# Optimization experiments

Measured on AMD Instinct MI355X. Metric: run time of the kernel, lower is better.

Reference implementation:

```python
import jax, jax.numpy as jnp
import numpy as np

HID = 256
STYLE_DIM = 64
NUM_STYLES = 8
IN_DIM = 3 + STYLE_DIM


def setup_inputs() -> dict:
    key = jax.random.key(0)
    ks = jax.random.split(key, 12)
    B, H, W = 2, 512, 512
    rgb = jax.random.uniform(ks[0], (B, 3, H, W), dtype=jnp.float32)
    style_idx = jax.random.randint(ks[1], (B,), 0, NUM_STYLES, dtype=jnp.int32)
    # style embedding table (torch init: normal std=0.01)
    emb_table = 0.01 * jax.random.normal(ks[2], (NUM_STYLES, STYLE_DIM), dtype=jnp.float32)
    # kaiming-normal (fan_in, relu gain sqrt(2)) weights stored as [in, out]
    def kaiming(k, fan_in, fan_out):
        std = np.sqrt(2.0 / fan_in)
        return std * jax.random.normal(k, (fan_in, fan_out), dtype=jnp.float32)
    W0 = kaiming(ks[3], IN_DIM, HID); b0 = jnp.zeros((HID,), jnp.float32)
    W1 = kaiming(ks[4], HID, HID);    b1 = jnp.zeros((HID,), jnp.float32)
    W2 = kaiming(ks[5], HID, HID);    b2 = jnp.zeros((HID,), jnp.float32)
    W3 = kaiming(ks[6], HID, 3);      b3 = jnp.zeros((3,), jnp.float32)
    return {"rgb": rgb, "style_idx": style_idx, "emb_table": emb_table,
            "W0": W0, "b0": b0, "W1": W1, "b1": b1,
            "W2": W2, "b2": b2, "W3": W3, "b3": b3}


def reference(rgb, style_idx, emb_table, W0, b0, W1, b1, W2, b2, W3, b3):
    B, C, H, W_ = rgb.shape  # CHW image input
    # [B,3,H,W] -> [B*H*W, 3]
    rgb_flat = jnp.transpose(rgb, (0, 2, 3, 1)).reshape(-1, 3)
    # style embedding lookup, broadcast per pixel
    emb = emb_table[style_idx]                              # [B, style_dim]
    emb = jnp.broadcast_to(emb[:, None, :], (B, H * W_, STYLE_DIM)).reshape(-1, STYLE_DIM)
    x = jnp.concatenate([rgb_flat, emb], axis=-1)           # [N, 67]
    gelu = lambda t: jax.nn.gelu(t, approximate=False)      # torch nn.GELU default (erf)
    x = gelu(x @ W0 + b0)
    x = gelu(x @ W1 + b1)
    x = gelu(x @ W2 + b2)
    out_flat = jax.nn.sigmoid(x @ W3 + b3)                  # [N, 3]
    out = out_flat.reshape(B, H, W_, 3).transpose(0, 3, 1, 2)
    return out
```

## Files before the change

kernel.cpp:

```cpp
#include <hip/hip_runtime.h>

#define HW  (512*512)

typedef _Float16 half8  __attribute__((__vector_size__(16)));
typedef _Float16 half4  __attribute__((__vector_size__(8)));
typedef _Float16 half2_t __attribute__((__vector_size__(4)));
typedef float    floatx4 __attribute__((__vector_size__(16)));
typedef float    floatx2 __attribute__((__vector_size__(8)));

__device__ __forceinline__ float gelu_f(float x){
    float x2 = x * x;
    float q  = __builtin_fmaf(x2, -0.1029432f, -2.3022079f);
    float e  = __builtin_amdgcn_exp2f(x * q);
    return x * __builtin_amdgcn_rcpf(1.0f + e);
}

__device__ __forceinline__ float sigmoid_f(float x){
    float e = __builtin_amdgcn_exp2f(-1.44269504f * x);
    return __builtin_amdgcn_rcpf(1.0f + e);
}

__device__ __forceinline__ float glut_eval(const float* gl, float x){
    float p = __builtin_fmaf(x, 128.0f, 1024.0f);
    p = fminf(fmaxf(p, 0.0f), 2040.0f);
    unsigned off = ((unsigned)p) & 0xFFFFFFF8u;
    floatx2 ab = *(const floatx2*)((const char*)gl + off);
    return __builtin_fmaf(ab[0], x, ab[1]);
}


__global__ void prep_all(const float* __restrict__ W1, const float* __restrict__ W2,
                         const float* __restrict__ W3, const float* __restrict__ emb,
                         const int* __restrict__ sidx, const float* __restrict__ W0,
                         const float* __restrict__ b0,
                         _Float16* __restrict__ wp, float* __restrict__ c0){
    __shared__ float ld[32][68];
    int blk = blockIdx.x;
    int tid = threadIdx.x;
    if (blk < 64){
        int mat = blk >> 5;
        int g   = blk & 31;
        int ks  = g >> 2;
        int ntq = g & 3;
        const float* W = mat ? W2 : W1;
        int row = tid >> 3;
        int c8  = (tid & 7) * 8;
        const float* src = &W[(ks*32 + row)*256 + ntq*64 + c8];
        *(floatx4*)&ld[row][c8]     = *(const floatx4*)src;
        *(floatx4*)&ld[row][c8 + 4] = *(const floatx4*)(src + 4);
        __syncthreads();
        int lane = tid & 63;
        int nt_l = tid >> 6;
        half8 h;
        #pragma unroll
        for (int j = 0; j < 8; j++)
            h[j] = (_Float16)ld[(lane >> 4)*8 + j][nt_l*16 + (lane & 15)];
        _Float16* dst = wp + mat*65536 + (ks*16 + ntq*4 + nt_l)*512 + lane*8;
        *(half8*)dst = h;
    } else if (blk < 80){
        int i    = (blk - 64)*256 + tid;
        int j    = i & 7;
        int lane = (i >> 3) & 63;
        int ks   = i >> 9;
        int k = ks*32 + ((lane >> 4) << 3) + j;
        int n = lane & 15;
        wp[131072 + i] = (_Float16)((n < 3) ? W3[k*3 + n] : 0.0f);
    } else {
        int b = blk - 80;
        int s = sidx[b];
        float acc = b0[tid];
        #pragma unroll 8
        for (int d = 0; d < 64; d++)
            acc = fmaf(emb[s*64 + d], W0[(3 + d)*256 + tid], acc);
        c0[b*256 + tid] = acc;
    }
}

__global__ __launch_bounds__(256, 4)
void nilut_main(const float* __restrict__ rgb,
                const float* __restrict__ W0,
                const float* __restrict__ b1v,
                const float* __restrict__ b2v,
                const float* __restrict__ b3v,
                const _Float16* __restrict__ wp,
                const float* __restrict__ c0,
                float* __restrict__ out){
    __shared__ __align__(16) _Float16 act[64 * 256];
    __shared__ __align__(16) float    w0s[1024];
    __shared__ __align__(16) float    rgbs[192];
    __shared__ __align__(16) float    glut[512];

    const int tid = threadIdx.x;
    const int wg  = blockIdx.x;
    const int pixbase = wg * 64;
    const int b   = pixbase >> 18;
    const int hw0 = pixbase & (HW - 1);

    #pragma unroll
    for (int r = 0; r < 4; r++){
        int q = r*256 + tid;
        w0s[q ^ ((q >> 4) & 6)] = (q < 768) ? W0[q] : c0[b*256 + (q - 768)];
    }
    if (tid < 192){
        int c = tid >> 6, row = tid & 63;
        rgbs[tid] = rgb[b*3*HW + c*HW + hw0 + row];
    }
    {
        float x0 = -8.0f + (float)tid * 0.0625f;
        float g0 = gelu_f(x0);
        float g1 = gelu_f(x0 + 0.0625f);
        float a  = (g1 - g0) * 16.0f;
        float bb = __builtin_fmaf(-a, x0, g0);
        floatx2 ab = {a, bb};
        *(floatx2*)&glut[2*tid] = ab;
    }
    __syncthreads();

    {
        int ng = tid & 31;
        int rg = tid >> 5;
        int s2 = (ng >> 2) & 3;
        floatx2 cw2[4][4];
        #pragma unroll
        for (int p = 0; p < 4; p++){
            const float* bp = &w0s[p*256 + ng*8];
            #pragma unroll
            for (int q = 0; q < 4; q++)
                cw2[p][q] = *(const floatx2*)&bp[2*(q ^ s2)];
        }
        #pragma unroll
        for (int hf = 0; hf < 2; hf++){
            floatx4 rv[3];
            #pragma unroll
            for (int c = 0; c < 3; c++)
                rv[c] = *(const floatx4*)&rgbs[c*64 + rg*8 + hf*4];
            #pragma unroll
            for (int r4 = 0; r4 < 4; r4++){
                int row = rg*8 + hf*4 + r4;
                floatx2 rr2 = {rv[0][r4], rv[0][r4]};
                floatx2 gg2 = {rv[1][r4], rv[1][r4]};
                floatx2 bb2 = {rv[2][r4], rv[2][r4]};
                half8 v;
                #pragma unroll
                for (int j2 = 0; j2 < 4; j2++){
                    floatx2 z2 = rr2*cw2[0][j2] + (gg2*cw2[1][j2] + (bb2*cw2[2][j2] + cw2[3][j2]));
                    half2_t g = __builtin_amdgcn_cvt_pkrtz(gelu_f(z2[0]), gelu_f(z2[1]));
                    v[2*j2]   = g[0];
                    v[2*j2+1] = g[1];
                }
                *(half8*)&act[row*256 + ((ng ^ (row & 7)) << 3)] = v;
            }
        }
    }
    __syncthreads();

    const int lane = tid & 63;
    const int wv   = tid >> 6;
    const int ln15 = lane & 15;
    const int quad = lane >> 4;
    const int qr   = quad * 4;
    const int sx   = ln15 & 7;
    const int qx8  = (quad ^ (sx & 3)) * 8;
    const int kb32 = ((sx >> 2) & 1) << 5;

    int pbq[4];
    #pragma unroll
    for (int pt = 0; pt < 4; pt++)
        pbq[pt] = (pt*16 + ln15)*256 + qx8;

    const int qh = quad >> 1, qs = (quad & 1) * 4;
    int eb[4];
    #pragma unroll
    for (int pt = 0; pt < 4; pt++)
        eb[pt] = (pt*16 + ln15)*256 + qs;

    const _Float16* wl  = wp;
    const float* bias   = b1v;
    #pragma unroll 1
    for (int L = 0; L < 2; L++){
        floatx4 acc[4][4];
        #pragma unroll
        for (int mtl = 0; mtl < 4; mtl++){
            floatx4 bv = *(const floatx4*)&bias[(wv*4 + mtl)*16 + qr];
            #pragma unroll
            for (int pt = 0; pt < 4; pt++)
                acc[pt][mtl] = bv;
        }

        const half8* wp8 = (const half8*)wl;
        #pragma unroll 2
        for (int ks = 0; ks < 8; ks++){
            int t = (ks << 5) ^ kb32;
            half8 bfr[4];
            #pragma unroll
            for (int pt = 0; pt < 4; pt++)
                bfr[pt] = *(const half8*)&act[pbq[pt] + t];
            #pragma unroll
            for (int mtl = 0; mtl < 4; mtl++){
                half8 af = wp8[(ks*16 + wv*4 + mtl)*64 + lane];
                #pragma unroll
                for (int pt = 0; pt < 4; pt++)
                    acc[pt][mtl] = __builtin_amdgcn_mfma_f32_16x16x32_f16(af, bfr[pt], acc[pt][mtl], 0, 0, 0);
            }
        }
        __syncthreads();
        #pragma unroll
        for (int mtl = 0; mtl < 4; mtl++){
            int cx = (((wv*4 + mtl)*2 + qh) ^ sx) << 3;
            #pragma unroll
            for (int pt = 0; pt < 4; pt++){
                floatx4 v = acc[pt][mtl];
                half2_t g01 = __builtin_amdgcn_cvt_pkrtz(glut_eval(glut, v[0]),
                                                         glut_eval(glut, v[1]));
                half2_t g23 = __builtin_amdgcn_cvt_pkrtz(glut_eval(glut, v[2]),
                                                         glut_eval(glut, v[3]));
                half4 h;
                h[0] = g01[0]; h[1] = g01[1]; h[2] = g23[0]; h[3] = g23[1];
                *(half4*)&act[eb[pt] + cx] = h;
            }
        }
        __syncthreads();
        wl = wp + 65536;
        bias = b2v;
    }

    {
        const half8* wp8 = (const half8*)(wp + 131072);
        floatx4 ac = (floatx4){0.f,0.f,0.f,0.f};
        int pb = (wv*16 + ln15)*256 + qx8;
        #pragma unroll
        for (int ks = 0; ks < 8; ks++){
            half8 bfr = *(const half8*)&act[pb + ((ks << 5) ^ kb32)];
            half8 af  = wp8[ks*64 + lane];
            ac = __builtin_amdgcn_mfma_f32_16x16x32_f16(af, bfr, ac, 0, 0, 0);
        }
        if (quad == 0){
            #pragma unroll
            for (int r = 0; r < 3; r++)
                w0s[r*64 + wv*16 + ln15] = sigmoid_f(ac[r] + b3v[r]);
        }
        __syncthreads();
        if (tid < 48){
            int c  = tid >> 4;
            int i2 = tid & 15;
            float4* dst = (float4*)(out + (b*3 + c)*HW + hw0);
            dst[i2] = ((float4*)(w0s + c*64))[i2];
        }
    }
}

extern "C" void kernel_launch(void* const* d_in, const int* in_sizes, int n_in,
                              void* d_out, int out_size, void* d_ws, size_t ws_size,
                              hipStream_t stream){
    const float* rgb = (const float*)d_in[0];
    const int*  sidx = (const int*) d_in[1];
    const float* emb = (const float*)d_in[2];
    const float* W0  = (const float*)d_in[3];
    const float* b0  = (const float*)d_in[4];
    const float* W1  = (const float*)d_in[5];
    const float* b1  = (const float*)d_in[6];
    const float* W2  = (const float*)d_in[7];
    const float* b2  = (const float*)d_in[8];
    const float* W3  = (const float*)d_in[9];
    const float* b3  = (const float*)d_in[10];
    float* out = (float*)d_out;

    _Float16* wp = (_Float16*)d_ws;
    float*    c0 = (float*)((char*)d_ws + 270336);

    int n_pix = in_sizes[0] / 3;
    prep_all<<<82, 256, 0, stream>>>(W1, W2, W3, emb, sidx, W0, b0, wp, c0);
    nilut_main<<<n_pix / 64, 256, 0, stream>>>(rgb, W0, b1, b2, b3, wp, c0, out);
}
```

Baseline: 258.7 us.

## Make workgroups persistent over eight 64-pixel tiles with prefetched RGB

Each workgroup now loops over eight consecutive 64-pixel tiles instead of one, so the W0/c0 staging and the GELU lookup table are built once per eight tiles. The RGB values for the next tile are loaded into registers during the current tile's compute. The first layer now uses the piecewise-linear GELU lookup instead of the exp-based GELU, and outputs go through a separate shared buffer. The grid shrinks to 1024 workgroups, which reduces parallel slack across CUs and hard-codes the pixel count.

```diff
diff --git a/kernel.cpp b/kernel.cpp
--- a/kernel.cpp
+++ b/kernel.cpp
@@ -88,22 +88,19 @@
     __shared__ __align__(16) _Float16 act[64 * 256];
     __shared__ __align__(16) float    w0s[1024];
     __shared__ __align__(16) float    rgbs[192];
+    __shared__ __align__(16) float    obounce[192];
     __shared__ __align__(16) float    glut[512];
 
     const int tid = threadIdx.x;
     const int wg  = blockIdx.x;
-    const int pixbase = wg * 64;
-    const int b   = pixbase >> 18;
-    const int hw0 = pixbase & (HW - 1);
+    const int b   = wg >> 9;
+    const int hwbase = (wg & 511) * 512;
+    const float* rgb_b = rgb + b*3*HW;
 
     #pragma unroll
     for (int r = 0; r < 4; r++){
         int q = r*256 + tid;
         w0s[q ^ ((q >> 4) & 6)] = (q < 768) ? W0[q] : c0[b*256 + (q - 768)];
-    }
-    if (tid < 192){
-        int c = tid >> 6, row = tid & 63;
-        rgbs[tid] = rgb[b*3*HW + c*HW + hw0 + row];
     }
     {
         float x0 = -8.0f + (float)tid * 0.0625f;
@@ -114,46 +111,15 @@
         floatx2 ab = {a, bb};
         *(floatx2*)&glut[2*tid] = ab;
     }
-    __syncthreads();
-
-    {
-        int ng = tid & 31;
-        int rg = tid >> 5;
-        int s2 = (ng >> 2) & 3;
-        floatx2 cw2[4][4];
-        #pragma unroll
-        for (int p = 0; p < 4; p++){
-            const float* bp = &w0s[p*256 + ng*8];
-            #pragma unroll
-            for (int q = 0; q < 4; q++)
-                cw2[p][q] = *(const floatx2*)&bp[2*(q ^ s2)];
-        }
-        #pragma unroll
-        for (int hf = 0; hf < 2; hf++){
-            floatx4 rv[3];
-            #pragma unroll
-            for (int c = 0; c < 3; c++)
-                rv[c] = *(const floatx4*)&rgbs[c*64 + rg*8 + hf*4];
-            #pragma unroll
-            for (int r4 = 0; r4 < 4; r4++){
-                int row = rg*8 + hf*4 + r4;
-                floatx2 rr2 = {rv[0][r4], rv[0][r4]};
-                floatx2 gg2 = {rv[1][r4], rv[1][r4]};
-                floatx2 bb2 = {rv[2][r4], rv[2][r4]};
-                half8 v;
-                #pragma unroll
-                for (int j2 = 0; j2 < 4; j2++){
-                    floatx2 z2 = rr2*cw2[0][j2] + (gg2*cw2[1][j2] + (bb2*cw2[2][j2] + cw2[3][j2]));
-                    half2_t g = __builtin_amdgcn_cvt_pkrtz(gelu_f(z2[0]), gelu_f(z2[1]));
-                    v[2*j2]   = g[0];
-                    v[2*j2+1] = g[1];
-                }
-                *(half8*)&act[row*256 + ((ng ^ (row & 7)) << 3)] = v;
-            }
-        }
-    }
-    __syncthreads();
-
+    const int rgb_c   = tid >> 6;
+    const int rgb_row = tid & 63;
+    const int rgb_off = rgb_c*HW + rgb_row;
+    if (tid < 192)
+        rgbs[tid] = rgb_b[rgb_off + hwbase];
+
+    const int ng = tid & 31;
+    const int rg = tid >> 5;
+    const int s2 = (ng >> 2) & 3;
     const int lane = tid & 63;
     const int wv   = tid >> 6;
     const int ln15 = lane & 15;
@@ -163,88 +129,134 @@
     const int qx8  = (quad ^ (sx & 3)) * 8;
     const int kb32 = ((sx >> 2) & 1) << 5;
 
-    int pbq[4];
+    int pbq[4], eb[4];
+    const int qh = quad >> 1, qs = (quad & 1) * 4;
     #pragma unroll
-    for (int pt = 0; pt < 4; pt++)
+    for (int pt = 0; pt < 4; pt++){
         pbq[pt] = (pt*16 + ln15)*256 + qx8;
-
-    const int qh = quad >> 1, qs = (quad & 1) * 4;
-    int eb[4];
-    #pragma unroll
-    for (int pt = 0; pt < 4; pt++)
-        eb[pt] = (pt*16 + ln15)*256 + qs;
-
-    const _Float16* wl  = wp;
-    const float* bias   = b1v;
+        eb[pt]  = (pt*16 + ln15)*256 + qs;
+    }
+    const int pbf = (wv*16 + ln15)*256 + qx8;
+
     #pragma unroll 1
-    for (int L = 0; L < 2; L++){
-        floatx4 acc[4][4];
-        #pragma unroll
-        for (int mtl = 0; mtl < 4; mtl++){
-            floatx4 bv = *(const floatx4*)&bias[(wv*4 + mtl)*16 + qr];
-            #pragma unroll
-            for (int pt = 0; pt < 4; pt++)
-                acc[pt][mtl] = bv;
-        }
-
-        const half8* wp8 = (const half8*)wl;
-        #pragma unroll 2
-        for (int ks = 0; ks < 8; ks++){
-            int t = (ks << 5) ^ kb32;
-            half8 bfr[4];
-            #pragma unroll
-            for (int pt = 0; pt < 4; pt++)
-                bfr[pt] = *(const half8*)&act[pbq[pt] + t];
-            #pragma unroll
-            for (int mtl = 0; mtl < 4; mtl++){
-                half8 af = wp8[(ks*16 + wv*4 + mtl)*64 + lane];
-                #pragma unroll
-                for (int pt = 0; pt < 4; pt++)
-                    acc[pt][mtl] = __builtin_amdgcn_mfma_f32_16x16x32_f16(af, bfr[pt], acc[pt][mtl], 0, 0, 0);
+    for (int it = 0; it < 8; ++it){
+        const int hw0 = hwbase + it*64;
+        __syncthreads();
+
+        float rnext = 0.0f;
+        if (it < 7 && tid < 192)
+            rnext = rgb_b[rgb_off + hw0 + 64];
+
+        {
+            floatx2 cw2[4][4];
+            #pragma unroll
+            for (int p = 0; p < 4; p++){
+                const float* bp = &w0s[p*256 + ng*8];
+                #pragma unroll
+                for (int q = 0; q < 4; q++)
+                    cw2[p][q] = *(const floatx2*)&bp[2*(q ^ s2)];
+            }
+            #pragma unroll
+            for (int hf = 0; hf < 2; hf++){
+                floatx4 rv[3];
+                #pragma unroll
+                for (int c = 0; c < 3; c++)
+                    rv[c] = *(const floatx4*)&rgbs[c*64 + rg*8 + hf*4];
+                #pragma unroll
+                for (int r4 = 0; r4 < 4; r4++){
+                    int row = rg*8 + hf*4 + r4;
+                    floatx2 rr2 = {rv[0][r4], rv[0][r4]};
+                    floatx2 gg2 = {rv[1][r4], rv[1][r4]};
+                    floatx2 bb2 = {rv[2][r4], rv[2][r4]};
+                    half8 v;
+                    #pragma unroll
+                    for (int j2 = 0; j2 < 4; j2++){
+                        floatx2 z2 = rr2*cw2[0][j2] + (gg2*cw2[1][j2] + (bb2*cw2[2][j2] + cw2[3][j2]));
+                        half2_t g = __builtin_amdgcn_cvt_pkrtz(glut_eval(glut, z2[0]),
+                                                               glut_eval(glut, z2[1]));
+                        v[2*j2]   = g[0];
+                        v[2*j2+1] = g[1];
+                    }
+                    *(half8*)&act[row*256 + ((ng ^ (row & 7)) << 3)] = v;
+                }
             }
         }
         __syncthreads();
-        #pragma unroll
-        for (int mtl = 0; mtl < 4; mtl++){
-            int cx = (((wv*4 + mtl)*2 + qh) ^ sx) << 3;
-            #pragma unroll
-            for (int pt = 0; pt < 4; pt++){
-                floatx4 v = acc[pt][mtl];
-                half2_t g01 = __builtin_amdgcn_cvt_pkrtz(glut_eval(glut, v[0]),
-                                                         glut_eval(glut, v[1]));
-                half2_t g23 = __builtin_amdgcn_cvt_pkrtz(glut_eval(glut, v[2]),
-                                                         glut_eval(glut, v[3]));
-                half4 h;
-                h[0] = g01[0]; h[1] = g01[1]; h[2] = g23[0]; h[3] = g23[1];
-                *(half4*)&act[eb[pt] + cx] = h;
-            }
+
+        if (it < 7 && tid < 192)
+            rgbs[tid] = rnext;
+
+        const _Float16* wl  = wp;
+        const float* bias   = b1v;
+        #pragma unroll 1
+        for (int L = 0; L < 2; L++){
+            floatx4 acc[4][4];
+            #pragma unroll
+            for (int mtl = 0; mtl < 4; mtl++){
+                floatx4 bv = *(const floatx4*)&bias[(wv*4 + mtl)*16 + qr];
+                #pragma unroll
+                for (int pt = 0; pt < 4; pt++)
+                    acc[pt][mtl] = bv;
+            }
+
+            const half8* wp8 = (const half8*)wl;
+            #pragma unroll 2
+            for (int ks = 0; ks < 8; ks++){
+                int t = (ks << 5) ^ kb32;
+                half8 bfr[4];
+                #pragma unroll
+                for (int pt = 0; pt < 4; pt++)
+                    bfr[pt] = *(const half8*)&act[pbq[pt] + t];
+                #pragma unroll
+                for (int mtl = 0; mtl < 4; mtl++){
+                    half8 af = wp8[(ks*16 + wv*4 + mtl)*64 + lane];
+                    #pragma unroll
+                    for (int pt = 0; pt < 4; pt++)
+                        acc[pt][mtl] = __builtin_amdgcn_mfma_f32_16x16x32_f16(af, bfr[pt], acc[pt][mtl], 0, 0, 0);
+                }
+            }
+            __syncthreads();
+            #pragma unroll
+            for (int mtl = 0; mtl < 4; mtl++){
+                int cx = (((wv*4 + mtl)*2 + qh) ^ sx) << 3;
+                #pragma unroll
+                for (int pt = 0; pt < 4; pt++){
+                    floatx4 v = acc[pt][mtl];
+                    half2_t g01 = __builtin_amdgcn_cvt_pkrtz(glut_eval(glut, v[0]),
+                                                             glut_eval(glut, v[1]));
+                    half2_t g23 = __builtin_amdgcn_cvt_pkrtz(glut_eval(glut, v[2]),
+                                                             glut_eval(glut, v[3]));
+                    half4 h;
+                    h[0] = g01[0]; h[1] = g01[1]; h[2] = g23[0]; h[3] = g23[1];
+                    *(half4*)&act[eb[pt] + cx] = h;
+                }
+            }
+            __syncthreads();
+            wl = wp + 65536;
+            bias = b2v;
         }
-        __syncthreads();
-        wl = wp + 65536;
-        bias = b2v;
-    }
-
-    {
-        const half8* wp8 = (const half8*)(wp + 131072);
-        floatx4 ac = (floatx4){0.f,0.f,0.f,0.f};
-        int pb = (wv*16 + ln15)*256 + qx8;
-        #pragma unroll
-        for (int ks = 0; ks < 8; ks++){
-            half8 bfr = *(const half8*)&act[pb + ((ks << 5) ^ kb32)];
-            half8 af  = wp8[ks*64 + lane];
-            ac = __builtin_amdgcn_mfma_f32_16x16x32_f16(af, bfr, ac, 0, 0, 0);
-        }
-        if (quad == 0){
-            #pragma unroll
-            for (int r = 0; r < 3; r++)
-                w0s[r*64 + wv*16 + ln15] = sigmoid_f(ac[r] + b3v[r]);
-        }
-        __syncthreads();
-        if (tid < 48){
-            int c  = tid >> 4;
-            int i2 = tid & 15;
-            float4* dst = (float4*)(out + (b*3 + c)*HW + hw0);
-            dst[i2] = ((float4*)(w0s + c*64))[i2];
+
+        {
+            const half8* wp8 = (const half8*)(wp + 131072);
+            floatx4 ac = (floatx4){0.f,0.f,0.f,0.f};
+            #pragma unroll
+            for (int ks = 0; ks < 8; ks++){
+                half8 bfr = *(const half8*)&act[pbf + ((ks << 5) ^ kb32)];
+                half8 af  = wp8[ks*64 + lane];
+                ac = __builtin_amdgcn_mfma_f32_16x16x32_f16(af, bfr, ac, 0, 0, 0);
+            }
+            if (quad == 0){
+                #pragma unroll
+                for (int r = 0; r < 3; r++)
+                    obounce[r*64 + wv*16 + ln15] = sigmoid_f(ac[r] + b3v[r]);
+            }
+            __syncthreads();
+            if (tid < 48){
+                int c  = tid >> 4;
+                int i2 = tid & 15;
+                float4* dst = (float4*)(out + (b*3 + c)*HW + hw0);
+                dst[i2] = ((float4*)(obounce + c*64))[i2];
+            }
         }
     }
 }
@@ -268,7 +280,6 @@
     _Float16* wp = (_Float16*)d_ws;
     float*    c0 = (float*)((char*)d_ws + 270336);
 
-    int n_pix = in_sizes[0] / 3;
     prep_all<<<82, 256, 0, stream>>>(W1, W2, W3, emb, sidx, W0, b0, wp, c0);
-    nilut_main<<<n_pix / 64, 256, 0, stream>>>(rgb, W0, b1, b2, b3, wp, c0, out);
-}
+    nilut_main<<<1024, 256, 0, stream>>>(rgb, W0, b1, b2, b3, wp, c0, out);
+}
```

After: 350.4 us. 1.35x slower.
